# Kernel tuning notes

Measured on AMD Instinct MI355X. Metric: run time of the kernel, lower is better.

The kernel has to match this reference:

```python
import jax, jax.numpy as jnp
import numpy as np

B, L, D, H, MAXS = 32, 2048, 1024, 16, 10
DH = D // H

def _ln(x, w, b, eps=1e-5):
    mu = jnp.mean(x, axis=-1, keepdims=True)
    var = jnp.var(x, axis=-1, keepdims=True)
    return (x - mu) * jax.lax.rsqrt(var + eps) * w + b

def setup_inputs() -> dict:
    key = jax.random.key(0)
    ks = jax.random.split(key, 6)
    s = 1.0 / np.sqrt(D)
    return {
        "grid_embeddings": jax.random.normal(ks[0], (B, L, D), dtype=jnp.float32),
        "symbol_queries": jax.random.normal(ks[1], (MAXS, D), dtype=jnp.float32) * 0.02,
        "qn_w": jnp.ones((D,), jnp.float32), "qn_b": jnp.zeros((D,), jnp.float32),
        "in_proj_w": jax.random.uniform(ks[2], (3 * D, D), jnp.float32, -s, s),
        "in_proj_b": jnp.zeros((3 * D,), jnp.float32),
        "out_w": jax.random.uniform(ks[3], (D, D), jnp.float32, -s, s),
        "out_b": jnp.zeros((D,), jnp.float32),
        "on_w": jnp.ones((D,), jnp.float32), "on_b": jnp.zeros((D,), jnp.float32),
        "symbol_position": 3,
    }

def reference(grid_embeddings, symbol_queries, qn_w, qn_b, in_proj_w, in_proj_b,
              out_w, out_b, on_w, on_b, symbol_position):
    Wq, Wk, Wv = in_proj_w[:D], in_proj_w[D:2*D], in_proj_w[2*D:]
    bq, bk, bv = in_proj_b[:D], in_proj_b[D:2*D], in_proj_b[2*D:]
    # query is identical across batch: compute once
    q0 = _ln(symbol_queries[symbol_position], qn_w, qn_b)          # [D]
    q = (q0 @ Wq.T + bq).reshape(H, DH)                             # [H, DH]
    k = (grid_embeddings @ Wk.T + bk).reshape(B, L, H, DH)          # [B, L, H, DH]
    v = (grid_embeddings @ Wv.T + bv).reshape(B, L, H, DH)          # [B, L, H, DH]
    scale = 1.0 / np.sqrt(DH).astype(np.float32)
    scores = jnp.einsum('hd,blhd->bhl', q, k) * scale               # [B, H, L]
    attn = jax.nn.softmax(scores, axis=-1)                          # [B, H, L]
    ctx = jnp.einsum('bhl,blhd->bhd', attn, v).reshape(B, D)        # [B, D]
    pooled = _ln(ctx @ out_w.T + out_b, on_w, on_b)                 # [B, D]
    return pooled, attn[:, :, None, :]                              # [B,H,1,L]
```

## Files before the change

kernel.cpp:

```cpp
#include <hip/hip_runtime.h>
#include <hip/hip_bf16.h>
#include <math.h>

#define BB 32
#define LL 2048
#define DD 1024
#define HH 16
#define DHH 64
#define NCK 16
#define CH  128
#define NT  8

#define WS_Q     1024
#define WS_R     2048
#define WS_C     18432
#define WS_CTX   19008
#define WS_Y     51776
#define WS_SSUM  84544
#define WS_PART  92736

#define RED_OFF  65536
#define WT_OFF   73728
#define SMEM_BYTES 77824

typedef __attribute__((ext_vector_type(8))) short    bf16x8;
typedef __attribute__((ext_vector_type(4))) short    bf16x4;
typedef __attribute__((ext_vector_type(4))) float    f32x4;
typedef __attribute__((ext_vector_type(2))) unsigned u32x2;
typedef __attribute__((ext_vector_type(4))) unsigned short u16x4;

#define MFMA(a, b, c) __builtin_amdgcn_mfma_f32_16x16x32_bf16(a, b, c, 0, 0, 0)

#if defined(__has_builtin)
#if __has_builtin(__builtin_amdgcn_mfma_f32_16x16x16bf16_1k)
#define HAVE_MFMA16 1
#define MFMA16(a, b, c) __builtin_amdgcn_mfma_f32_16x16x16bf16_1k(a, b, c, 0, 0, 0)
#endif
#endif
#ifndef HAVE_MFMA16
#define HAVE_MFMA16 0
#endif

__device__ __forceinline__ unsigned short f2bf(float f) {
    unsigned u = __float_as_uint(f);
    return (unsigned short)((u + 0x7FFFu + ((u >> 16) & 1u)) >> 16);
}
__device__ __forceinline__ u16x4 pk4(float4 f) {
    __hip_bfloat162 a = __float22bfloat162_rn(make_float2(f.x, f.y));
    __hip_bfloat162 b = __float22bfloat162_rn(make_float2(f.z, f.w));
    ushort2 ua = *reinterpret_cast<ushort2*>(&a);
    ushort2 ub = *reinterpret_cast<ushort2*>(&b);
    u16x4 r; r[0] = ua.x; r[1] = ua.y; r[2] = ub.x; r[3] = ub.y;
    return r;
}
__device__ __forceinline__ float bf2f(unsigned short u) {
    return __uint_as_float((unsigned)u << 16);
}
__device__ __forceinline__ float wave_sum(float v) {
#pragma unroll
    for (int s = 32; s >= 1; s >>= 1) v += __shfl_xor(v, s, 64);
    return v;
}

__global__ void k_q(const float* __restrict__ sq, const float* __restrict__ qn_w,
                    const float* __restrict__ qn_b, const int* __restrict__ pos,
                    const float* __restrict__ ipw, const float* __restrict__ ipb,
                    float* __restrict__ ws) {
    const int t = threadIdx.x;
    const int w = t >> 6, lane = t & 63;
    __shared__ float q0s[DD];
    __shared__ float rs[4], rs2[4];
    {
        const float4 x = ((const float4*)(sq + (size_t)pos[0] * DD))[t];
        float s  = x.x + x.y + x.z + x.w;
        float s2 = x.x * x.x + x.y * x.y + x.z * x.z + x.w * x.w;
        s = wave_sum(s); s2 = wave_sum(s2);
        if (lane == 0) { rs[w] = s; rs2[w] = s2; }
        __syncthreads();
        s  = rs[0] + rs[1] + rs[2] + rs[3];
        s2 = rs2[0] + rs2[1] + rs2[2] + rs2[3];
        const float mu  = s * (1.0f / DD);
        const float var = s2 * (1.0f / DD) - mu * mu;
        const float rstd = rsqrtf(var + 1e-5f);
        const float4 w4 = ((const float4*)qn_w)[t];
        const float4 b4 = ((const float4*)qn_b)[t];
        float4 o;
        o.x = (x.x - mu) * rstd * w4.x + b4.x;
        o.y = (x.y - mu) * rstd * w4.y + b4.y;
        o.z = (x.z - mu) * rstd * w4.z + b4.z;
        o.w = (x.w - mu) * rstd * w4.w + b4.w;
        ((float4*)q0s)[t] = o;
    }
    __syncthreads();
    const int d = blockIdx.x * 4 + w;
    const float* row = ipw + (size_t)d * DD;
    float acc = 0.f;
#pragma unroll
    for (int it = 0; it < 4; ++it) {
        float4 a = ((const float4*)row)[lane + 64 * it];
        float4 b = ((const float4*)q0s)[lane + 64 * it];
        acc += a.x * b.x + a.y * b.y + a.z * b.z + a.w * b.w;
    }
    acc = wave_sum(acc);
    if (lane == 0) (ws + WS_Q)[d] = acc + ipb[d];
}

__global__ void k_r(const float* __restrict__ ipw, const float* __restrict__ ipb,
                    float* __restrict__ ws) {
    const int h = blockIdx.x >> 4, s = blockIdx.x & 15;
    const int t = threadIdx.x;
    const int e = s * 64 + t;
    const float* q = ws + WS_Q;
    const float* wk = ipw + (size_t)(DD + h * DHH) * DD;
    float acc = 0.f;
#pragma unroll 8
    for (int j = 0; j < DHH; ++j)
        acc += q[h * DHH + j] * wk[(size_t)j * DD + e];
    (ws + WS_R)[h * DD + e] = acc * 0.125f;
    if (s == 0) {
        float p = q[h * DHH + t] * ipb[DD + h * DHH + t];
        p = wave_sum(p);
        if (t == 0) (ws + WS_C)[h] = p * 0.125f;
    }
}

__global__ __launch_bounds__(512, 4)
void k_fused(const float* __restrict__ gr, const float* __restrict__ ws,
             float* __restrict__ attn_e, unsigned short* __restrict__ part,
             float* __restrict__ ssum) {
    extern __shared__ char smem[];
    const int b  = blockIdx.x >> 4;
    const int ck = blockIdx.x & 15;
    const int l0 = ck * CH;
    const int t  = threadIdx.x;
    const int wv = t >> 6, lane = t & 63;
    const int c16 = lane & 15, g = lane >> 4;
    const int estrip = wv * 128;

    bf16x8 rpk[4];
#pragma unroll
    for (int ks = 0; ks < 4; ++ks) {
        const float* rp = ws + WS_R + (size_t)c16 * DD + estrip + ks * 32 + g * 8;
        float4 f0 = *(const float4*)rp, f1 = *(const float4*)(rp + 4);
        u16x4 lo = pk4(f0), hi = pk4(f1);
        bf16x8 r;
        r[0] = (short)lo[0]; r[1] = (short)lo[1]; r[2] = (short)lo[2]; r[3] = (short)lo[3];
        r[4] = (short)hi[0]; r[5] = (short)hi[1]; r[6] = (short)hi[2]; r[7] = (short)hi[3];
        rpk[ks] = r;
    }
    const float myc = (ws + WS_C)[c16];

    f32x4 pv[8];
#pragma unroll
    for (int i = 0; i < 8; ++i) pv[i] = (f32x4){0.f, 0.f, 0.f, 0.f};
    float s_acc = 0.f;

    const int srow = ((lane >> 2) & 3) + (wv & 3) * 4;
    const int se0  = (lane & 3) * 4 + ((lane >> 4) + (wv >> 2) * 4) * 16;
    const float* gbase = gr + ((size_t)(b * LL + l0) + srow) * DD + se0;
    const int wr_base = ((lane >> 4) + (wv >> 2) * 4) * 512 + (wv & 3) * 128 +
                        ((lane >> 2) & 3) * 32 + (lane & 3) * 8;

    float4 raw[8];
#pragma unroll
    for (int j = 0; j < 8; ++j) raw[j] = *(const float4*)(gbase + 128 * j);
#pragma unroll
    for (int j = 0; j < 8; ++j)
        *(u16x4*)(smem + wr_base + j * 4096) = pk4(raw[j]);
#pragma unroll
    for (int j = 0; j < 8; ++j)
        raw[j] = *(const float4*)(gbase + 16 * DD + 128 * j);
    __syncthreads();

#pragma unroll 1
    for (int tt = 0; tt < NT; ++tt) {
        const char* rb = smem + (tt & 1) * 32768;
        f32x4 sa = {0.f, 0.f, 0.f, 0.f};
#pragma unroll
        for (int ks = 0; ks < 4; ++ks) {
            const int e16 = wv * 8 + ks * 2 + (g >> 1);
            const int byt = (e16 * 4 + (c16 >> 2)) * 128 + (c16 & 3) * 32 + (g & 1) * 16;
            bf16x8 a = *(const bf16x8*)(rb + byt);
            sa = MFMA(a, rpk[ks], sa);
        }
        *(f32x4*)(smem + RED_OFF + (wv * 64 + lane) * 16) = sa;
        __syncthreads();
        if (tt < NT - 1) {
            char* wb = smem + ((tt + 1) & 1) * 32768;
#pragma unroll
            for (int j = 0; j < 8; ++j)
                *(u16x4*)(wb + wr_base + j * 4096) = pk4(raw[j]);
            if (tt < NT - 2) {
                const float* gs = gbase + (size_t)(tt + 2) * 16 * DD;
#pragma unroll
                for (int j = 0; j < 8; ++j)
                    raw[j] = *(const float4*)(gs + 128 * j);
            }
        }
        f32x4 tot = {myc, myc, myc, myc};
#pragma unroll
        for (int w2 = 0; w2 < 8; ++w2)
            tot += *(const f32x4*)(smem + RED_OFF + (w2 * 64 + lane) * 16);
        f32x4 ex;
        ex[0] = __expf(tot[0]); ex[1] = __expf(tot[1]);
        ex[2] = __expf(tot[2]); ex[3] = __expf(tot[3]);
        *(u16x4*)(smem + WT_OFF + wv * 512 + c16 * 32 + g * 8) =
            pk4(make_float4(ex[0], ex[1], ex[2], ex[3]));
        if (wv == (tt & 7)) {
            float* ap = attn_e + ((size_t)b * HH + c16) * LL + l0 + tt * 16 + g * 4;
            *(float4*)ap = make_float4(ex[0], ex[1], ex[2], ex[3]);
        }
        s_acc += ex[0] + ex[1] + ex[2] + ex[3];
#if HAVE_MFMA16
        bf16x4 afrag;
        {
            u16x4 aw = *(const u16x4*)(smem + WT_OFF + wv * 512 + c16 * 32 + g * 8);
            afrag[0] = (short)aw[0]; afrag[1] = (short)aw[1];
            afrag[2] = (short)aw[2]; afrag[3] = (short)aw[3];
        }
        {
            u32x2 q[8];
#pragma unroll
            for (int nt = 0; nt < 8; ++nt) {
                const int est = wv * 8 + nt;
                const unsigned ta = (unsigned)((tt & 1) * 32768 + est * 512 +
                                               g * 128 + c16 * 8);
                asm volatile("ds_read_b64_tr_b16 %0, %1"
                             : "=v"(q[nt]) : "v"(ta));
            }
            asm volatile("s_waitcnt lgkmcnt(0)" ::: "memory");
            __builtin_amdgcn_sched_barrier(0);
#pragma unroll
            for (int nt = 0; nt < 8; ++nt) {
                union { unsigned u[2]; bf16x4 v; } bb;
                bb.u[0] = q[nt][0]; bb.u[1] = q[nt][1];
                pv[nt] = MFMA16(afrag, bb.v, pv[nt]);
            }
        }
#else
        bf16x8 afrag;
        if (g < 2) {
            afrag = *(const bf16x8*)(smem + WT_OFF + wv * 512 + c16 * 32 + g * 16);
        } else {
            afrag = (bf16x8){0, 0, 0, 0, 0, 0, 0, 0};
        }
#pragma unroll
        for (int grp = 0; grp < 2; ++grp) {
            u32x2 q[8];
#pragma unroll
            for (int n2 = 0; n2 < 4; ++n2) {
                const int est = wv * 8 + grp * 4 + n2;
                const unsigned ta = (unsigned)((tt & 1) * 32768 + est * 512 +
                                               (g & 1) * 256 + c16 * 8);
                asm volatile("ds_read_b64_tr_b16 %0, %1"
                             : "=v"(q[n2 * 2]) : "v"(ta));
                asm volatile("ds_read_b64_tr_b16 %0, %1 offset:128"
                             : "=v"(q[n2 * 2 + 1]) : "v"(ta));
            }
            asm volatile("s_waitcnt lgkmcnt(0)" ::: "memory");
            __builtin_amdgcn_sched_barrier(0);
#pragma unroll
            for (int n2 = 0; n2 < 4; ++n2) {
                union { unsigned u[4]; bf16x8 v; } bb;
                bb.u[0] = q[n2 * 2][0];     bb.u[1] = q[n2 * 2][1];
                bb.u[2] = q[n2 * 2 + 1][0]; bb.u[3] = q[n2 * 2 + 1][1];
                pv[grp * 4 + n2] = MFMA(afrag, bb.v, pv[grp * 4 + n2]);
            }
        }
#endif
        __syncthreads();
    }
    float sv = s_acc;
    sv += __shfl_xor(sv, 16, 64);
    sv += __shfl_xor(sv, 32, 64);
    if (wv == 0 && lane < 16)
        ssum[((size_t)b * NCK + ck) * HH + c16] = sv;
    unsigned short* pp = part + ((size_t)b * NCK + ck) * (HH * DD);
#pragma unroll
    for (int nt = 0; nt < 8; ++nt) {
#pragma unroll
        for (int r2 = 0; r2 < 4; ++r2)
            pp[(size_t)(g * 4 + r2) * DD + estrip + nt * 16 + c16] = f2bf(pv[nt][r2]);
    }
}

__global__ void k_ctx(const float* __restrict__ ipw, const float* __restrict__ ipb,
                      const unsigned short* __restrict__ part,
                      const float* __restrict__ ssum,
                      float* __restrict__ attn_e, float* __restrict__ ctx) {
    const int bh = blockIdx.x, b = bh >> 4, h = bh & 15;
    const int t = threadIdx.x, w = t >> 6, lane = t & 63;
    float S = 0.f;
#pragma unroll
    for (int c = 0; c < NCK; ++c) S += ssum[((size_t)b * NCK + c) * HH + h];
    const float inv = 1.0f / S;
    float4* ar = (float4*)(attn_e + (size_t)bh * LL);
#pragma unroll
    for (int i = 0; i < 2; ++i) {
        float4 v = ar[t + 256 * i];
        v.x *= inv; v.y *= inv; v.z *= inv; v.w *= inv;
        ar[t + 256 * i] = v;
    }
    __shared__ float Xl[DD];
    float4 x = {0.f, 0.f, 0.f, 0.f};
#pragma unroll
    for (int c = 0; c < NCK; ++c) {
        u16x4 p = *(const u16x4*)(part + ((size_t)b * NCK + c) * (HH * DD) +
                                  (size_t)h * DD + t * 4);
        x.x += bf2f(p[0]); x.y += bf2f(p[1]);
        x.z += bf2f(p[2]); x.w += bf2f(p[3]);
    }
    float4 xs = {x.x * inv, x.y * inv, x.z * inv, x.w * inv};
    ((float4*)Xl)[t] = xs;
    __syncthreads();
    for (int jj = 0; jj < 16; ++jj) {
        const int j = w * 16 + jj;
        const float* row = ipw + (size_t)(2 * DD + h * DHH + j) * DD;
        float acc = 0.f;
#pragma unroll
        for (int it = 0; it < 4; ++it) {
            float4 a = ((const float4*)row)[lane + 64 * it];
            float4 p = ((const float4*)Xl)[lane + 64 * it];
            acc += a.x * p.x + a.y * p.y + a.z * p.z + a.w * p.w;
        }
        acc = wave_sum(acc);
        if (lane == 0) ctx[(size_t)b * DD + h * DHH + j] = acc + ipb[2 * DD + h * DHH + j];
    }
}

__global__ void k_y(const float* __restrict__ ow, const float* __restrict__ ob,
                    const float* __restrict__ ctx, float* __restrict__ y) {
    const int blk = blockIdx.x, b = blk >> 4, ch = blk & 15;
    const int t = threadIdx.x, w = t >> 6, lane = t & 63;
    __shared__ float Xl[DD];
    ((float4*)Xl)[t] = ((const float4*)(ctx + (size_t)b * DD))[t];
    __syncthreads();
    for (int jj = 0; jj < 16; ++jj) {
        const int d = ch * 64 + w * 16 + jj;
        const float* row = ow + (size_t)d * DD;
        float acc = 0.f;
#pragma unroll
        for (int it = 0; it < 4; ++it) {
            float4 a = ((const float4*)row)[lane + 64 * it];
            float4 p = ((const float4*)Xl)[lane + 64 * it];
            acc += a.x * p.x + a.y * p.y + a.z * p.z + a.w * p.w;
        }
        acc = wave_sum(acc);
        if (lane == 0) y[(size_t)b * DD + d] = acc + ob[d];
    }
}

__global__ void k_lnout(const float* __restrict__ y, const float* __restrict__ on_w,
                        const float* __restrict__ on_b, float* __restrict__ outp) {
    const int b = blockIdx.x, t = threadIdx.x;
    const float4 x = ((const float4*)(y + (size_t)b * DD))[t];
    float s  = x.x + x.y + x.z + x.w;
    float s2 = x.x * x.x + x.y * x.y + x.z * x.z + x.w * x.w;
    __shared__ float rs[4], rs2[4];
    s = wave_sum(s); s2 = wave_sum(s2);
    const int w = t >> 6, lane = t & 63;
    if (lane == 0) { rs[w] = s; rs2[w] = s2; }
    __syncthreads();
    s  = rs[0] + rs[1] + rs[2] + rs[3];
    s2 = rs2[0] + rs2[1] + rs2[2] + rs2[3];
    const float mu  = s * (1.0f / DD);
    const float var = s2 * (1.0f / DD) - mu * mu;
    const float rstd = rsqrtf(var + 1e-5f);
    const float4 w4 = ((const float4*)on_w)[t];
    const float4 b4 = ((const float4*)on_b)[t];
    float4 o;
    o.x = (x.x - mu) * rstd * w4.x + b4.x;
    o.y = (x.y - mu) * rstd * w4.y + b4.y;
    o.z = (x.z - mu) * rstd * w4.z + b4.z;
    o.w = (x.w - mu) * rstd * w4.w + b4.w;
    ((float4*)(outp + (size_t)b * DD))[t] = o;
}

extern "C" void kernel_launch(void* const* d_in, const int* in_sizes, int n_in,
                              void* d_out, int out_size, void* d_ws, size_t ws_size,
                              hipStream_t stream) {
    const float* gr   = (const float*)d_in[0];
    const float* sq   = (const float*)d_in[1];
    const float* qn_w = (const float*)d_in[2];
    const float* qn_b = (const float*)d_in[3];
    const float* ipw  = (const float*)d_in[4];
    const float* ipb  = (const float*)d_in[5];
    const float* ow   = (const float*)d_in[6];
    const float* ob   = (const float*)d_in[7];
    const float* on_w = (const float*)d_in[8];
    const float* on_b = (const float*)d_in[9];
    const int*   pos  = (const int*)d_in[10];

    float* out  = (float*)d_out;
    float* attn = out + BB * DD;
    float* ws   = (float*)d_ws;
    unsigned short* part16 = (unsigned short*)(ws + WS_PART);

    hipFuncSetAttribute((const void*)k_fused,
                        hipFuncAttributeMaxDynamicSharedMemorySize, SMEM_BYTES);

    k_q<<<256, 256, 0, stream>>>(sq, qn_w, qn_b, pos, ipw, ipb, ws);
    k_r<<<256, 64, 0, stream>>>(ipw, ipb, ws);
    k_fused<<<BB * NCK, 512, SMEM_BYTES, stream>>>(gr, ws, attn,
                                                   part16, ws + WS_SSUM);
    k_ctx<<<BB * HH, 256, 0, stream>>>(ipw, ipb, part16, ws + WS_SSUM,
                                       attn, ws + WS_CTX);
    k_y<<<BB * 16, 256, 0, stream>>>(ow, ob, ws + WS_CTX, ws + WS_Y);
    k_lnout<<<BB, 256, 0, stream>>>(ws + WS_Y, on_w, on_b, out);
}
```

Measured before the change: 100.1 us.

## Software-pipeline score MFMA across tiles and drop one barrier per iteration

Each wave now computes the score partials for the next tile at the end of the current iteration. The partials go into a double-buffered reduction area, so each tile needs one __syncthreads instead of two. Global loads of the grid tile are remapped so each wave stages exactly the element strip it later reads, which makes the LDS traffic wave-local. The per-wave score partials are also stored in bf16 to halve reduction traffic. That adds rounding before the exp and could hurt the accuracy of the attention output.

```diff
diff --git a/kernel.cpp b/kernel.cpp
--- a/kernel.cpp
+++ b/kernel.cpp
@@ -52,6 +52,9 @@
     ushort2 ub = *reinterpret_cast<ushort2*>(&b);
     u16x4 r; r[0] = ua.x; r[1] = ua.y; r[2] = ub.x; r[3] = ub.y;
     return r;
+}
+__device__ __forceinline__ u16x4 pk4v(f32x4 f) {
+    return pk4(make_float4(f[0], f[1], f[2], f[3]));
 }
 __device__ __forceinline__ float bf2f(unsigned short u) {
     return __uint_as_float((unsigned)u << 16);
@@ -155,70 +158,72 @@
     for (int i = 0; i < 8; ++i) pv[i] = (f32x4){0.f, 0.f, 0.f, 0.f};
     float s_acc = 0.f;
 
-    const int srow = ((lane >> 2) & 3) + (wv & 3) * 4;
-    const int se0  = (lane & 3) * 4 + ((lane >> 4) + (wv >> 2) * 4) * 16;
-    const float* gbase = gr + ((size_t)(b * LL + l0) + srow) * DD + se0;
-    const int wr_base = ((lane >> 4) + (wv >> 2) * 4) * 512 + (wv & 3) * 128 +
+    const int srow = (lane >> 4) * 4 + ((lane >> 2) & 3);
+    const float* gbase = gr + ((size_t)(b * LL + l0) + srow) * DD +
+                         estrip + (lane & 3) * 4;
+    const int wr_base = (wv * 8) * 512 + (lane >> 4) * 128 +
                         ((lane >> 2) & 3) * 32 + (lane & 3) * 8;
 
+
     float4 raw[8];
 #pragma unroll
-    for (int j = 0; j < 8; ++j) raw[j] = *(const float4*)(gbase + 128 * j);
+    for (int j = 0; j < 8; ++j) raw[j] = *(const float4*)(gbase + 16 * j);
 #pragma unroll
     for (int j = 0; j < 8; ++j)
-        *(u16x4*)(smem + wr_base + j * 4096) = pk4(raw[j]);
+        *(u16x4*)(smem + wr_base + j * 512) = pk4(raw[j]);
 #pragma unroll
     for (int j = 0; j < 8; ++j)
-        raw[j] = *(const float4*)(gbase + 16 * DD + 128 * j);
-    __syncthreads();
-
-#pragma unroll 1
-    for (int tt = 0; tt < NT; ++tt) {
-        const char* rb = smem + (tt & 1) * 32768;
+        raw[j] = *(const float4*)(gbase + 16 * DD + 16 * j);
+    {
         f32x4 sa = {0.f, 0.f, 0.f, 0.f};
 #pragma unroll
         for (int ks = 0; ks < 4; ++ks) {
             const int e16 = wv * 8 + ks * 2 + (g >> 1);
             const int byt = (e16 * 4 + (c16 >> 2)) * 128 + (c16 & 3) * 32 + (g & 1) * 16;
-            bf16x8 a = *(const bf16x8*)(rb + byt);
+            bf16x8 a = *(const bf16x8*)(smem + byt);
             sa = MFMA(a, rpk[ks], sa);
         }
-        *(f32x4*)(smem + RED_OFF + (wv * 64 + lane) * 16) = sa;
-        __syncthreads();
-        if (tt < NT - 1) {
-            char* wb = smem + ((tt + 1) & 1) * 32768;
-#pragma unroll
-            for (int j = 0; j < 8; ++j)
-                *(u16x4*)(wb + wr_base + j * 4096) = pk4(raw[j]);
-            if (tt < NT - 2) {
-                const float* gs = gbase + (size_t)(tt + 2) * 16 * DD;
-#pragma unroll
-                for (int j = 0; j < 8; ++j)
-                    raw[j] = *(const float4*)(gs + 128 * j);
-            }
-        }
+        *(u16x4*)(smem + RED_OFF + (wv * 64 + lane) * 8) = pk4v(sa);
+    }
+    __syncthreads();
+
+#pragma unroll 1
+    for (int tt = 0; tt < NT; ++tt) {
         f32x4 tot = {myc, myc, myc, myc};
 #pragma unroll
-        for (int w2 = 0; w2 < 8; ++w2)
-            tot += *(const f32x4*)(smem + RED_OFF + (w2 * 64 + lane) * 16);
+        for (int w2 = 0; w2 < 8; ++w2) {
+            u16x4 p = *(const u16x4*)(smem + RED_OFF + (tt & 1) * 4096 +
+                                      (w2 * 64 + lane) * 8);
+            tot[0] += bf2f(p[0]); tot[1] += bf2f(p[1]);
+            tot[2] += bf2f(p[2]); tot[3] += bf2f(p[3]);
+        }
         f32x4 ex;
         ex[0] = __expf(tot[0]); ex[1] = __expf(tot[1]);
         ex[2] = __expf(tot[2]); ex[3] = __expf(tot[3]);
-        *(u16x4*)(smem + WT_OFF + wv * 512 + c16 * 32 + g * 8) =
-            pk4(make_float4(ex[0], ex[1], ex[2], ex[3]));
+        *(u16x4*)(smem + WT_OFF + wv * 512 + c16 * 32 + g * 8) = pk4v(ex);
         if (wv == (tt & 7)) {
             float* ap = attn_e + ((size_t)b * HH + c16) * LL + l0 + tt * 16 + g * 4;
             *(float4*)ap = make_float4(ex[0], ex[1], ex[2], ex[3]);
         }
         s_acc += ex[0] + ex[1] + ex[2] + ex[3];
+        if (tt < NT - 1) {
+            char* wb = smem + ((tt + 1) & 1) * 32768;
+#pragma unroll
+            for (int j = 0; j < 8; ++j)
+                *(u16x4*)(wb + wr_base + j * 512) = pk4(raw[j]);
+            if (tt < NT - 2) {
+                const float* gs = gbase + (size_t)(tt + 2) * 16 * DD;
+#pragma unroll
+                for (int j = 0; j < 8; ++j)
+                    raw[j] = *(const float4*)(gs + 16 * j);
+            }
+        }
 #if HAVE_MFMA16
-        bf16x4 afrag;
         {
+            bf16x4 afrag;
             u16x4 aw = *(const u16x4*)(smem + WT_OFF + wv * 512 + c16 * 32 + g * 8);
             afrag[0] = (short)aw[0]; afrag[1] = (short)aw[1];
             afrag[2] = (short)aw[2]; afrag[3] = (short)aw[3];
-        }
-        {
             u32x2 q[8];
 #pragma unroll
             for (int nt = 0; nt < 8; ++nt) {
@@ -238,36 +243,51 @@
             }
         }
 #else
-        bf16x8 afrag;
-        if (g < 2) {
-            afrag = *(const bf16x8*)(smem + WT_OFF + wv * 512 + c16 * 32 + g * 16);
-        } else {
-            afrag = (bf16x8){0, 0, 0, 0, 0, 0, 0, 0};
-        }
-#pragma unroll
-        for (int grp = 0; grp < 2; ++grp) {
-            u32x2 q[8];
-#pragma unroll
-            for (int n2 = 0; n2 < 4; ++n2) {
-                const int est = wv * 8 + grp * 4 + n2;
-                const unsigned ta = (unsigned)((tt & 1) * 32768 + est * 512 +
-                                               (g & 1) * 256 + c16 * 8);
-                asm volatile("ds_read_b64_tr_b16 %0, %1"
-                             : "=v"(q[n2 * 2]) : "v"(ta));
-                asm volatile("ds_read_b64_tr_b16 %0, %1 offset:128"
-                             : "=v"(q[n2 * 2 + 1]) : "v"(ta));
-            }
-            asm volatile("s_waitcnt lgkmcnt(0)" ::: "memory");
-            __builtin_amdgcn_sched_barrier(0);
-#pragma unroll
-            for (int n2 = 0; n2 < 4; ++n2) {
-                union { unsigned u[4]; bf16x8 v; } bb;
-                bb.u[0] = q[n2 * 2][0];     bb.u[1] = q[n2 * 2][1];
-                bb.u[2] = q[n2 * 2 + 1][0]; bb.u[3] = q[n2 * 2 + 1][1];
-                pv[grp * 4 + n2] = MFMA(afrag, bb.v, pv[grp * 4 + n2]);
+        {
+            bf16x8 afrag;
+            if (g < 2) {
+                afrag = *(const bf16x8*)(smem + WT_OFF + wv * 512 + c16 * 32 + g * 16);
+            } else {
+                afrag = (bf16x8){0, 0, 0, 0, 0, 0, 0, 0};
+            }
+#pragma unroll
+            for (int grp = 0; grp < 2; ++grp) {
+                u32x2 q[8];
+#pragma unroll
+                for (int n2 = 0; n2 < 4; ++n2) {
+                    const int est = wv * 8 + grp * 4 + n2;
+                    const unsigned ta = (unsigned)((tt & 1) * 32768 + est * 512 +
+                                                   (g & 1) * 256 + c16 * 8);
+                    asm volatile("ds_read_b64_tr_b16 %0, %1"
+                                 : "=v"(q[n2 * 2]) : "v"(ta));
+                    asm volatile("ds_read_b64_tr_b16 %0, %1 offset:128"
+                                 : "=v"(q[n2 * 2 + 1]) : "v"(ta));
+                }
+                asm volatile("s_waitcnt lgkmcnt(0)" ::: "memory");
+                __builtin_amdgcn_sched_barrier(0);
+#pragma unroll
+                for (int n2 = 0; n2 < 4; ++n2) {
+                    union { unsigned u[4]; bf16x8 v; } bb;
+                    bb.u[0] = q[n2 * 2][0];     bb.u[1] = q[n2 * 2][1];
+                    bb.u[2] = q[n2 * 2 + 1][0]; bb.u[3] = q[n2 * 2 + 1][1];
+                    pv[grp * 4 + n2] = MFMA(afrag, bb.v, pv[grp * 4 + n2]);
+                }
             }
         }
 #endif
+        if (tt < NT - 1) {
+            const char* rb = smem + ((tt + 1) & 1) * 32768;
+            f32x4 sa = {0.f, 0.f, 0.f, 0.f};
+#pragma unroll
+            for (int ks = 0; ks < 4; ++ks) {
+                const int e16 = wv * 8 + ks * 2 + (g >> 1);
+                const int byt = (e16 * 4 + (c16 >> 2)) * 128 + (c16 & 3) * 32 + (g & 1) * 16;
+                bf16x8 a = *(const bf16x8*)(rb + byt);
+                sa = MFMA(a, rpk[ks], sa);
+            }
+            *(u16x4*)(smem + RED_OFF + ((tt + 1) & 1) * 4096 +
+                      (wv * 64 + lane) * 8) = pk4v(sa);
+        }
         __syncthreads();
     }
     float sv = s_acc;
```

After: 99.69 us. About the same (-0.4%).
